# Kernel tuning notes

Measured on AMD Instinct MI355X. Metric: run time of the kernel, lower is better.

Reference implementation:

```python
import jax, jax.numpy as jnp
import numpy as np

E, H, D = 512, 8, 64
B, T = 2, 1024
HD = H * D


def _linear(x, W, b):
    return x @ W + b


def _ln(x, g, b):
    mu = x.mean(-1, keepdims=True)
    var = ((x - mu) ** 2).mean(-1, keepdims=True)
    return (x - mu) / jnp.sqrt(var + 1e-5) * g + b


def _l2norm(x):
    n = jnp.sqrt((x * x).sum(-1, keepdims=True))
    return x / jnp.maximum(n, 1e-12)


def setup_inputs() -> dict:
    key = jax.random.key(0)
    ks = jax.random.split(key, 32)
    s = 0.02
    inp = {
        'x': jax.random.normal(ks[0], (B, T, E), jnp.float32),
        'b_min': jax.random.normal(ks[1], (B, T, E), jnp.float32),
        'b_max': jax.random.normal(ks[2], (B, T, E), jnp.float32),
        'motif_context': jax.random.normal(ks[3], (B, T, E), jnp.float32),
        'Wk': jax.random.normal(ks[4], (E, HD), jnp.float32) * s,
        'bk': jnp.zeros((HD,), jnp.float32),
        'Wq': jax.random.normal(ks[5], (E, HD), jnp.float32) * s,
        'bq': jnp.zeros((HD,), jnp.float32),
        'Wv': jax.random.normal(ks[6], (E, HD), jnp.float32) * s,
        'bv': jnp.zeros((HD,), jnp.float32),
        'Wo': jax.random.normal(ks[7], (HD, E), jnp.float32) * s,
        'bo': jnp.zeros((E,), jnp.float32),
        'Wd': jax.random.normal(ks[8], (E, H), jnp.float32) * s,
        'bd': jnp.zeros((H,), jnp.float32),
        'Wgw': jax.random.normal(ks[9], (E, H), jnp.float32) * s,
        'bgw': jnp.zeros((H,), jnp.float32),
        'Wgf': jax.random.normal(ks[10], (E, H), jnp.float32) * s,
        'bgf': jnp.zeros((H,), jnp.float32),
        'Wps': jax.random.normal(ks[11], (E, E), jnp.float32) * s,
        'bps': jnp.zeros((E,), jnp.float32),
        'ln1_g': jnp.ones((E,), jnp.float32),
        'ln1_b': jnp.zeros((E,), jnp.float32),
        'ln2_g': jnp.ones((E,), jnp.float32),
        'ln2_b': jnp.zeros((E,), jnp.float32),
        'W1': jax.random.normal(ks[12], (E, 4 * E), jnp.float32) * s,
        'b1': jnp.zeros((4 * E,), jnp.float32),
        'W2': jax.random.normal(ks[13], (4 * E, E), jnp.float32) * s,
        'b2': jnp.zeros((E,), jnp.float32),
    }
    return inp


def reference(x, b_min, b_max, motif_context,
              Wk, bk, Wq, bq, Wv, bv, Wo, bo, Wd, bd,
              Wgw, bgw, Wgf, bgf, Wps, bps,
              ln1_g, ln1_b, ln2_g, ln2_b, W1, b1, W2, b2):
    Bs, Ts, Es = x.shape
    x_n = _ln(x, ln1_g, ln1_b)
    k = _l2norm(_linear(x_n, Wk, bk).reshape(Bs, Ts, H, D))
    q = _l2norm(_linear(x_n, Wq, bq).reshape(Bs, Ts, H, D))
    v = jnp.tanh(_linear(x_n, Wv, bv).reshape(Bs, Ts, H, D))
    d = jax.nn.softplus(_linear(x_n, Wd, bd))            # (B,T,H)
    gw = jax.nn.sigmoid(_linear(x_n, Wgw, bgw)) ** 2     # (B,T,H)
    gf = 1.0 - jax.nn.sigmoid(_linear(x_n, Wgf, bgf)) ** 2

    # gated linear recurrent scan via cumsum of rank-1 updates
    v_gated = v * (d * gw)[..., None]                    # (B,T,H,D)
    updates = jnp.einsum('bthi,bthj->bthij', v_gated, k)  # (B,T,H,D,D)
    decay = jnp.clip(d * gf, 1e-6, 0.999)
    log_decay = jnp.log(decay)[..., None, None]          # (B,T,H,1,1)
    exp_cum_decay = jnp.exp(jnp.cumsum(log_decay, axis=1))
    state = jnp.cumsum(updates / (exp_cum_decay + 1e-8), axis=1) * exp_cum_decay
    readout = jnp.einsum('bthij,bthj->bthi', state, q)   # (B,T,H,D)
    next_mem = state[:, -1]

    x2 = x + _linear(readout.reshape(Bs, Ts, HD), Wo, bo) + 0.1 * motif_context
    h = _ln(x2, ln2_g, ln2_b)
    x3 = x2 + _linear(jax.nn.gelu(_linear(h, W1, b1), approximate=False), W2, b2)
    probe = _linear(x3, Wps, bps)
    return (x3, next_mem, b_min + probe, b_max + probe)
```

## Files before the change

kernel.cpp:

```cpp
#include <hip/hip_runtime.h>


typedef unsigned short u16;
typedef unsigned int u32;
typedef __attribute__((ext_vector_type(8))) short short8;
typedef __attribute__((ext_vector_type(4))) float floatx4;

__device__ __forceinline__ float b2f(u16 u) {
  u32 x = ((u32)u) << 16;
  return __uint_as_float(x);
}
__device__ __forceinline__ u16 f2b(float f) {
  u32 x = __float_as_uint(f);
  u32 r = (x + 0x7fffu + ((x >> 16) & 1u)) >> 16;
  return (u16)r;
}
__device__ __forceinline__ float4 b4_to_f4(uint2 u) {
  float4 r;
  r.x = __uint_as_float((u.x & 0xffffu) << 16);
  r.y = __uint_as_float(u.x & 0xffff0000u);
  r.z = __uint_as_float((u.y & 0xffffu) << 16);
  r.w = __uint_as_float(u.y & 0xffff0000u);
  return r;
}

__device__ __forceinline__ void stage16(const u16* g, u16* lds_wave_base) {
  __builtin_amdgcn_global_load_lds((const __attribute__((address_space(1))) void*)g,
                                   (__attribute__((address_space(3))) void*)lds_wave_base,
                                   16, 0, 0);
}

template <int ROWS>
__device__ __forceinline__ void stage_tile64(const u16* __restrict__ G, int ldK, int kb,
                                             u16* lds, int tid) {
#pragma unroll
  for (int r = 0; r < ROWS / 32; ++r) {
    int slot = r * 256 + tid;
    int row = slot >> 3;
    int kwg = (slot & 7) ^ (row & 7);
    stage16(G + (size_t)row * ldK + kb * 64 + kwg * 8,
            lds + (size_t)(r * 256 + (tid >> 6) * 64) * 8);
  }
}

__device__ __forceinline__ void ln_row(const float* __restrict__ xr,
                                       const float* __restrict__ g,
                                       const float* __restrict__ bt,
                                       u16* __restrict__ yr, int tid, float* red) {
  float x0 = xr[tid], x1 = xr[tid + 256];
  float s = x0 + x1, ss = x0 * x0 + x1 * x1;
#pragma unroll
  for (int o = 32; o > 0; o >>= 1) { s += __shfl_xor(s, o); ss += __shfl_xor(ss, o); }
  if ((tid & 63) == 0) { red[tid >> 6] = s; red[4 + (tid >> 6)] = ss; }
  __syncthreads();
  float ts = red[0] + red[1] + red[2] + red[3];
  float tss = red[4] + red[5] + red[6] + red[7];
  float mu = ts * (1.f / 512.f);
  float var = tss * (1.f / 512.f) - mu * mu;
  float rstd = 1.0f / sqrtf(var + 1e-5f);
  yr[tid] = f2b((x0 - mu) * rstd * g[tid] + bt[tid]);
  yr[tid + 256] = f2b((x1 - mu) * rstd * g[tid + 256] + bt[tid + 256]);
}

__global__ __launch_bounds__(256) void prep_weights(
    const float* __restrict__ Wk, const float* __restrict__ Wq,
    const float* __restrict__ Wv, const float* __restrict__ Wo,
    const float* __restrict__ Wps, const float* __restrict__ W1,
    const float* __restrict__ W2, const float* __restrict__ Wd,
    const float* __restrict__ Wgw, const float* __restrict__ Wgf,
    const float* __restrict__ bk, const float* __restrict__ bq,
    const float* __restrict__ bv, const float* __restrict__ bd,
    const float* __restrict__ bgw, const float* __restrict__ bgf,
    const float* __restrict__ x, const float* __restrict__ ln1g,
    const float* __restrict__ ln1b,
    u16* __restrict__ WTQ, u16* __restrict__ WTO, u16* __restrict__ WTPS,
    u16* __restrict__ WT1, u16* __restrict__ WT2, float* __restrict__ BQV,
    u16* __restrict__ XN) {
  int bid = blockIdx.x, tid = threadIdx.x;
  __shared__ float tile[32][33];
  __shared__ float red[8];
  if (bid < 3328) {
    const float* src;
    u16* dst;
    int C, rel, tiles_x;
    if (bid < 256)       { src = Wk;  dst = WTQ;           C = 512;  rel = bid;        tiles_x = 16; }
    else if (bid < 512)  { src = Wq;  dst = WTQ + 262144;  C = 512;  rel = bid - 256;  tiles_x = 16; }
    else if (bid < 768)  { src = Wv;  dst = WTQ + 524288;  C = 512;  rel = bid - 512;  tiles_x = 16; }
    else if (bid < 1024) { src = Wo;  dst = WTO;           C = 512;  rel = bid - 768;  tiles_x = 16; }
    else if (bid < 1280) { src = Wps; dst = WTPS;          C = 512;  rel = bid - 1024; tiles_x = 16; }
    else if (bid < 2304) { src = W1;  dst = WT1;           C = 2048; rel = bid - 1280; tiles_x = 64; }
    else                 { src = W2;  dst = WT2;           C = 512;  rel = bid - 2304; tiles_x = 16; }
    int R = (bid >= 1280 && bid < 2304) ? 512 : (bid >= 2304 ? 2048 : 512);
    int c0 = (rel % tiles_x) * 32, r0 = (rel / tiles_x) * 32;
    int tx = tid & 31, ty = tid >> 5;
#pragma unroll
    for (int i = 0; i < 4; ++i)
      tile[ty + i * 8][tx] = src[(size_t)(r0 + ty + i * 8) * C + c0 + tx];
    __syncthreads();
#pragma unroll
    for (int i = 0; i < 4; ++i)
      dst[(size_t)(c0 + ty + i * 8) * R + r0 + tx] = f2b(tile[tx][ty + i * 8]);
  } else if (bid < 3392) {
    int idx = (bid - 3328) * 256 + tid;
    const int stride = 64 * 256;
    for (int i = idx; i < 128 * 512; i += stride) {
      int local = i >> 9, k = i & 511;
      float v = 0.f;
      if (local < 8) v = Wd[k * 8 + local];
      else if (local < 16) v = Wgw[k * 8 + (local - 8)];
      else if (local < 24) v = Wgf[k * 8 + (local - 16)];
      WTQ[(size_t)(1536 + local) * 512 + k] = f2b(v);
    }
    for (int i = idx; i < 1664; i += stride) {
      float v = 0.f;
      if (i < 512) v = bk[i];
      else if (i < 1024) v = bq[i - 512];
      else if (i < 1536) v = bv[i - 1024];
      else if (i < 1544) v = bd[i - 1536];
      else if (i < 1552) v = bgw[i - 1544];
      else if (i < 1560) v = bgf[i - 1552];
      BQV[i] = v;
    }
  } else {
    int row = bid - 3392;
    ln_row(x + (size_t)row * 512, ln1g, ln1b, XN + (size_t)row * 512, tid, red);
  }
}

__global__ __launch_bounds__(256) void ln_f32(const float* __restrict__ X,
                                              const float* __restrict__ g,
                                              const float* __restrict__ bt,
                                              u16* __restrict__ Y) {
  __shared__ float red[8];
  ln_row(X + (size_t)blockIdx.x * 512, g, bt, Y + (size_t)blockIdx.x * 512,
         threadIdx.x, red);
}

template <int BM, int EPI>
__global__ __launch_bounds__(256, (BM == 64 ? 4 : 6)) void gemm2s(
    const u16* __restrict__ A, const u16* __restrict__ BT, const float* __restrict__ bias,
    float* __restrict__ outf, float* __restrict__ outf2, u16* __restrict__ outb,
    u16* __restrict__ outb2, u16* __restrict__ outb3,
    const float* __restrict__ aux0, const float* __restrict__ aux1, int M, int N, int K) {
  constexpr int MT = BM / 32;
  constexpr int S = BM / 32 + 2;
  __shared__ __align__(16) u16 As[2][BM * 64];
  __shared__ __align__(16) u16 Bs[2][64 * 64];
  __shared__ float ssb[2][BM];
  const int tid = threadIdx.x;
  const int lane = tid & 63, wave = tid >> 6;
  const int wm = wave >> 1, wn = wave & 1;
  const int m0 = blockIdx.y * BM, n0 = blockIdx.x * 64;
  floatx4 acc[MT][2] = {};
  const int fr = lane & 15, kq = lane >> 4;
  const int nk = K >> 6;
  const u16* Ab = A + (size_t)m0 * K;
  const u16* Bb = BT + (size_t)n0 * K;

  stage_tile64<BM>(Ab, K, 0, As[0], tid);
  stage_tile64<64>(Bb, K, 0, Bs[0], tid);

  for (int kb = 0; kb < nk; ++kb) {
    const int cur = kb & 1;
    if (kb + 1 < nk) {
      stage_tile64<BM>(Ab, K, kb + 1, As[cur ^ 1], tid);
      stage_tile64<64>(Bb, K, kb + 1, Bs[cur ^ 1], tid);
      if constexpr (S == 4) asm volatile("s_waitcnt vmcnt(4)" ::: "memory");
      else asm volatile("s_waitcnt vmcnt(3)" ::: "memory");
    } else {
      asm volatile("s_waitcnt vmcnt(0)" ::: "memory");
    }
    asm volatile("s_barrier" ::: "memory");

#pragma unroll
    for (int sub = 0; sub < 2; ++sub) {
      short8 af[MT], bf[2];
#pragma unroll
      for (int mt = 0; mt < MT; ++mt) {
        int row = wm * (BM / 2) + mt * 16 + fr;
        int c = sub * 4 + kq;
        af[mt] = *(const short8*)&As[cur][row * 64 + ((c ^ (row & 7)) << 3)];
      }
#pragma unroll
      for (int nt = 0; nt < 2; ++nt) {
        int row = wn * 32 + nt * 16 + fr;
        int c = sub * 4 + kq;
        bf[nt] = *(const short8*)&Bs[cur][row * 64 + ((c ^ (row & 7)) << 3)];
      }
#pragma unroll
      for (int mt = 0; mt < MT; ++mt)
#pragma unroll
        for (int nt = 0; nt < 2; ++nt)
          acc[mt][nt] =
              __builtin_amdgcn_mfma_f32_16x16x32_bf16(af[mt], bf[nt], acc[mt][nt], 0, 0, 0);
    }
    asm volatile("s_waitcnt lgkmcnt(0)" ::: "memory");
    asm volatile("s_barrier" ::: "memory");
  }

  const int col = lane & 15;
  const int rbase = (lane >> 4) * 4;

  float vv[MT][2][4];
#pragma unroll
  for (int nt = 0; nt < 2; ++nt) {
    int gc = n0 + wn * 32 + nt * 16 + col;
    float bvv = bias[gc];
#pragma unroll
    for (int mt = 0; mt < MT; ++mt)
#pragma unroll
      for (int r = 0; r < 4; ++r) vv[mt][nt][r] = acc[mt][nt][r] + bvv;
  }

  if constexpr (EPI == 5) {
    const int sec = n0 >> 9;
    const int h = (n0 & 511) >> 6;
    if (sec == 3) {
#pragma unroll
      for (int nt = 0; nt < 2; ++nt) {
        int gcl = (n0 - 1536) + wn * 32 + nt * 16 + col;
#pragma unroll
        for (int mt = 0; mt < MT; ++mt) {
          int gr = m0 + wm * (BM / 2) + mt * 16 + rbase;
#pragma unroll
          for (int r = 0; r < 4; ++r)
            outf[(size_t)(gr + r) * 128 + gcl] = vv[mt][nt][r];
        }
      }
    } else if (sec == 2) {
#pragma unroll
      for (int nt = 0; nt < 2; ++nt) {
        int d = wn * 32 + nt * 16 + col;
#pragma unroll
        for (int mt = 0; mt < MT; ++mt) {
          int gr = m0 + wm * (BM / 2) + mt * 16 + rbase;
#pragma unroll
          for (int r = 0; r < 4; ++r) {
            int tok = gr + r;
            int bh = (tok >> 10) * 8 + h;
            outb3[((size_t)bh * 1024 + (tok & 1023)) * 64 + d] = f2b(tanhf(vv[mt][nt][r]));
          }
        }
      }
    } else {
#pragma unroll
      for (int mt = 0; mt < MT; ++mt) {
#pragma unroll
        for (int r = 0; r < 4; ++r) {
          float ss = vv[mt][0][r] * vv[mt][0][r] + vv[mt][1][r] * vv[mt][1][r];
          ss += __shfl_xor(ss, 1);
          ss += __shfl_xor(ss, 2);
          ss += __shfl_xor(ss, 4);
          ss += __shfl_xor(ss, 8);
          if ((lane & 15) == 0)
            ssb[wn][wm * (BM / 2) + mt * 16 + rbase + r] = ss;
        }
      }
      __syncthreads();
      u16* dst = (sec == 0) ? outb : outb2;
#pragma unroll
      for (int mt = 0; mt < MT; ++mt) {
#pragma unroll
        for (int r = 0; r < 4; ++r) {
          int br = wm * (BM / 2) + mt * 16 + rbase + r;
          float tot = ssb[0][br] + ssb[1][br];
          float rs = 1.0f / fmaxf(sqrtf(tot), 1e-12f);
          int tok = m0 + br;
          int bh = (tok >> 10) * 8 + h;
          size_t base = ((size_t)bh * 1024 + (tok & 1023)) * 64;
#pragma unroll
          for (int nt = 0; nt < 2; ++nt) {
            int d = wn * 32 + nt * 16 + col;
            dst[base + d] = f2b(vv[mt][nt][r] * rs);
          }
        }
      }
    }
  } else {
#pragma unroll
    for (int nt = 0; nt < 2; ++nt) {
      int gc = n0 + wn * 32 + nt * 16 + col;
#pragma unroll
      for (int mt = 0; mt < MT; ++mt) {
        int gr = m0 + wm * (BM / 2) + mt * 16 + rbase;
#pragma unroll
        for (int r = 0; r < 4; ++r) {
          size_t idx = (size_t)(gr + r) * N + gc;
          float v = vv[mt][nt][r];
          if constexpr (EPI == 1) {
            outf[idx] = aux0[idx] + v + 0.1f * aux1[idx];
          } else if constexpr (EPI == 2) {
            outb[idx] = f2b(0.5f * v * (1.f + erff(v * 0.70710678118654752f)));
          } else if constexpr (EPI == 3) {
            float w = aux0[idx] + v;
            outf[idx] = w;
            outb[idx] = f2b(w);
          } else if constexpr (EPI == 4) {
            outf[idx] = aux0[idx] + v;
            outf2[idx] = aux1[idx] + v;
          }
        }
      }
    }
  }
}

__global__ __launch_bounds__(256) void gates_logcum(
    const float* __restrict__ G0, float* __restrict__ DEC, float* __restrict__ SVG,
    float* __restrict__ LC, float* __restrict__ WW) {
  int bh = blockIdx.x;
  int b = bh >> 3, h = bh & 7;
  int tid = threadIdx.x;
  __shared__ float ldec[1024];
#pragma unroll
  for (int tt = 0; tt < 4; ++tt) {
    int t = tt * 256 + tid;
    size_t tok = (size_t)b * 1024 + t;
    float dl = G0[tok * 128 + h];
    float gwl = G0[tok * 128 + 8 + h];
    float gfl = G0[tok * 128 + 16 + h];
    float dd = dl > 20.f ? dl : log1pf(expf(dl));
    float sw = 1.f / (1.f + expf(-gwl));
    float gw = sw * sw;
    float sf = 1.f / (1.f + expf(-gfl));
    float gf = 1.f - sf * sf;
    float dec = fminf(fmaxf(dd * gf, 1e-6f), 0.999f);
    ldec[t] = dec;
    DEC[(size_t)bh * 1024 + t] = dec;
    SVG[(size_t)bh * 1024 + t] = dd * gw;
  }
  __syncthreads();
  if (tid < 64) {
    int lane = tid;
    size_t base = (size_t)bh * 1024 + lane * 16;
    float loc[16];
    float run = 0.f;
#pragma unroll
    for (int i = 0; i < 16; ++i) { run += logf(ldec[lane * 16 + i]); loc[i] = run; }
    float x = run;
#pragma unroll
    for (int o = 1; o < 64; o <<= 1) {
      float v = __shfl_up(x, o);
      if (lane >= o) x += v;
    }
    float excl = x - run;
#pragma unroll
    for (int i = 0; i < 16; ++i) {
      float L = excl + loc[i];
      LC[base + i] = L;
      float c = expf(L);
      WW[base + i] = c / (c + 1e-8f);
    }
  }
}

__global__ __launch_bounds__(256, 2) void scan_phase1(
    const u16* __restrict__ KB, const u16* __restrict__ QB, const u16* __restrict__ VB,
    const float* __restrict__ DEC, const float* __restrict__ WW,
    const float* __restrict__ SVG, float* __restrict__ RP, float* __restrict__ SF) {
  int chunk = blockIdx.x, h = blockIdx.y, b = blockIdx.z;
  int bh = b * 8 + h;
  int t0 = chunk * 32;
  __shared__ __align__(16) float sk[2048], sq[2048], sv[2048];
  __shared__ float lsa[32], lsw[32];
  int tid = threadIdx.x;

  const u16* gk = KB + ((size_t)bh * 1024 + t0) * 64;
  const u16* gq = QB + ((size_t)bh * 1024 + t0) * 64;
  const u16* gv = VB + ((size_t)bh * 1024 + t0) * 64;
#pragma unroll
  for (int r = 0; r < 2; ++r) {
    int f = (r * 256 + tid) * 4;
    *(float4*)&sk[f] = b4_to_f4(*(const uint2*)(gk + f));
    *(float4*)&sq[f] = b4_to_f4(*(const uint2*)(gq + f));
    *(float4*)&sv[f] = b4_to_f4(*(const uint2*)(gv + f));
  }
  if (tid < 32) {
    size_t gi = (size_t)bh * 1024 + t0 + tid;
    lsa[tid] = DEC[gi];
    lsw[tid] = WW[gi] * SVG[gi];
  }
  __syncthreads();

  int i = tid >> 2, j0 = (tid & 3) * 16;
  float s[16];
#pragma unroll
  for (int z = 0; z < 16; ++z) s[z] = 0.f;

  for (int t = 0; t < 32; ++t) {
    float a = lsa[t], w = lsw[t];
    float wv = w * sv[t * 64 + i];
    float r = 0.f;
#pragma unroll
    for (int u4 = 0; u4 < 4; ++u4) {
      float4 kv = *(const float4*)&sk[t * 64 + j0 + u4 * 4];
      float4 qv = *(const float4*)&sq[t * 64 + j0 + u4 * 4];
      s[u4 * 4 + 0] = fmaf(a, s[u4 * 4 + 0], wv * kv.x); r = fmaf(s[u4 * 4 + 0], qv.x, r);
      s[u4 * 4 + 1] = fmaf(a, s[u4 * 4 + 1], wv * kv.y); r = fmaf(s[u4 * 4 + 1], qv.y, r);
      s[u4 * 4 + 2] = fmaf(a, s[u4 * 4 + 2], wv * kv.z); r = fmaf(s[u4 * 4 + 2], qv.z, r);
      s[u4 * 4 + 3] = fmaf(a, s[u4 * 4 + 3], wv * kv.w); r = fmaf(s[u4 * 4 + 3], qv.w, r);
    }
    r += __shfl_xor(r, 1);
    r += __shfl_xor(r, 2);
    if ((tid & 3) == 0)
      RP[((size_t)(b * 1024 + t0 + t) * 8 + h) * 64 + i] = r;
  }

  float* Sf = SF + ((size_t)bh * 32 + chunk) * 4096 + i * 64 + j0;
#pragma unroll
  for (int u4 = 0; u4 < 4; ++u4) {
    float4 v;
    v.x = s[u4 * 4 + 0]; v.y = s[u4 * 4 + 1]; v.z = s[u4 * 4 + 2]; v.w = s[u4 * 4 + 3];
    *(float4*)&Sf[u4 * 4] = v;
  }
}

__global__ __launch_bounds__(256) void scan_phase2p(const float* __restrict__ SF,
                                                    const float* __restrict__ LC,
                                                    float* __restrict__ SI,
                                                    float* __restrict__ next_mem) {
  int bh = blockIdx.x >> 4;
  int e = (blockIdx.x & 15) * 256 + threadIdx.x;
  float s = 0.f;
  for (int c = 0; c < 32; ++c) {
    SI[((size_t)bh * 32 + c) * 4096 + e] = s;
    float Lend = LC[(size_t)bh * 1024 + c * 32 + 31];
    float Lpre = c ? LC[(size_t)bh * 1024 + c * 32 - 1] : 0.f;
    float P = expf(Lend - Lpre);
    s = fmaf(P, s, SF[((size_t)bh * 32 + c) * 4096 + e]);
  }
  next_mem[(size_t)bh * 4096 + e] = s;
}

__global__ __launch_bounds__(256, 2) void scan_phase3(
    const u16* __restrict__ QB, const float* __restrict__ SI, const float* __restrict__ LC,
    const float* __restrict__ RP, u16* __restrict__ AB) {
  int chunk = blockIdx.x, h = blockIdx.y, b = blockIdx.z;
  int bh = b * 8 + h;
  int t0 = chunk * 32;
  __shared__ __align__(16) float sq[2048];
  __shared__ float sL[32];
  int tid = threadIdx.x;

  const u16* gq = QB + ((size_t)bh * 1024 + t0) * 64;
#pragma unroll
  for (int r = 0; r < 2; ++r) {
    int f = (r * 256 + tid) * 4;
    *(float4*)&sq[f] = b4_to_f4(*(const uint2*)(gq + f));
  }
  if (tid < 32) sL[tid] = LC[(size_t)bh * 1024 + t0 + tid];
  __syncthreads();

  float Lpre = chunk ? LC[(size_t)bh * 1024 + t0 - 1] : 0.f;
  int i = tid >> 2, j0 = (tid & 3) * 16;
  const float* Si = SI + ((size_t)bh * 32 + chunk) * 4096 + i * 64 + j0;
  float S[16];
#pragma unroll
  for (int u4 = 0; u4 < 4; ++u4) {
    float4 v = *(const float4*)&Si[u4 * 4];
    S[u4 * 4 + 0] = v.x; S[u4 * 4 + 1] = v.y; S[u4 * 4 + 2] = v.z; S[u4 * 4 + 3] = v.w;
  }

  for (int t = 0; t < 32; ++t) {
    float p = expf(sL[t] - Lpre);
    float r = 0.f;
#pragma unroll
    for (int u4 = 0; u4 < 4; ++u4) {
      float4 qv = *(const float4*)&sq[t * 64 + j0 + u4 * 4];
      r = fmaf(S[u4 * 4 + 0], qv.x, r);
      r = fmaf(S[u4 * 4 + 1], qv.y, r);
      r = fmaf(S[u4 * 4 + 2], qv.z, r);
      r = fmaf(S[u4 * 4 + 3], qv.w, r);
    }
    r += __shfl_xor(r, 1);
    r += __shfl_xor(r, 2);
    if ((tid & 3) == 0) {
      size_t gi = ((size_t)(b * 1024 + t0 + t) * 8 + h) * 64 + i;
      AB[gi] = f2b(RP[gi] + p * r);
    }
  }
}

extern "C" void kernel_launch(void* const* d_in, const int* in_sizes, int n_in,
                              void* d_out, int out_size, void* d_ws, size_t ws_size,
                              hipStream_t stream) {
  const float* x = (const float*)d_in[0];
  const float* bmin = (const float*)d_in[1];
  const float* bmax = (const float*)d_in[2];
  const float* motif = (const float*)d_in[3];
  const float* Wk = (const float*)d_in[4];
  const float* bk = (const float*)d_in[5];
  const float* Wq = (const float*)d_in[6];
  const float* bq = (const float*)d_in[7];
  const float* Wv = (const float*)d_in[8];
  const float* bv = (const float*)d_in[9];
  const float* Wo = (const float*)d_in[10];
  const float* bo = (const float*)d_in[11];
  const float* Wd = (const float*)d_in[12];
  const float* bd = (const float*)d_in[13];
  const float* Wgw = (const float*)d_in[14];
  const float* bgw = (const float*)d_in[15];
  const float* Wgf = (const float*)d_in[16];
  const float* bgf = (const float*)d_in[17];
  const float* Wps = (const float*)d_in[18];
  const float* bps = (const float*)d_in[19];
  const float* ln1g = (const float*)d_in[20];
  const float* ln1b = (const float*)d_in[21];
  const float* ln2g = (const float*)d_in[22];
  const float* ln2b = (const float*)d_in[23];
  const float* W1 = (const float*)d_in[24];
  const float* b1 = (const float*)d_in[25];
  const float* W2 = (const float*)d_in[26];
  const float* b2 = (const float*)d_in[27];

  char* ws = (char*)d_ws;
  u16* WTQ = (u16*)(ws + 0);
  u16* WTO = (u16*)(ws + 1703936);
  u16* WT1 = (u16*)(ws + 2228224);
  u16* WT2 = (u16*)(ws + 4325376);
  u16* WTPS = (u16*)(ws + 6422528);
  float* BQV = (float*)(ws + 6946816);
  u16* XN = (u16*)(ws + 6953984);
  float* G0 = (float*)(ws + 9051136);
  u16* KB = (u16*)(ws + 10099712);
  u16* QB = (u16*)(ws + 12196864);
  u16* VB = (u16*)(ws + 14294016);
  float* DEC = (float*)(ws + 16391168);
  float* LC = (float*)(ws + 16456704);
  float* WW = (float*)(ws + 16522240);
  float* SVG = (float*)(ws + 16587776);
  float* RP = (float*)(ws + 16653312);
  float* SF = (float*)(ws + 20847616);
  float* SI = (float*)(ws + 29236224);
  u16* AB = (u16*)(ws + 37624832);
  float* X2 = (float*)(ws + 39721984);
  u16* HB = (u16*)(ws + 43916288);
  u16* MID = (u16*)(ws + 9051136);
  u16* X3B = (u16*)(ws + 20847616);

  float* out0 = (float*)d_out;
  float* out1 = out0 + 1048576;
  float* out2 = out0 + 1114112;
  float* out3 = out0 + 2162688;

  prep_weights<<<5440, 256, 0, stream>>>(Wk, Wq, Wv, Wo, Wps, W1, W2, Wd, Wgw, Wgf,
                                         bk, bq, bv, bd, bgw, bgf, x, ln1g, ln1b,
                                         WTQ, WTO, WTPS, WT1, WT2, BQV, XN);
  gemm2s<64, 5><<<dim3(26, 32), 256, 0, stream>>>(XN, WTQ, BQV, G0, nullptr, KB, QB, VB,
                                                  nullptr, nullptr, 2048, 1664, 512);
  gates_logcum<<<16, 256, 0, stream>>>(G0, DEC, SVG, LC, WW);
  scan_phase1<<<dim3(32, 8, 2), 256, 0, stream>>>(KB, QB, VB, DEC, WW, SVG, RP, SF);
  scan_phase2p<<<256, 256, 0, stream>>>(SF, LC, SI, out1);
  scan_phase3<<<dim3(32, 8, 2), 256, 0, stream>>>(QB, SI, LC, RP, AB);

  gemm2s<32, 1><<<dim3(8, 64), 256, 0, stream>>>(AB, WTO, bo, X2, nullptr, nullptr,
                                                 nullptr, nullptr, x, motif, 2048, 512, 512);
  ln_f32<<<2048, 256, 0, stream>>>(X2, ln2g, ln2b, HB);
  gemm2s<64, 2><<<dim3(32, 32), 256, 0, stream>>>(HB, WT1, b1, nullptr, nullptr, MID,
                                                  nullptr, nullptr, nullptr, nullptr,
                                                  2048, 2048, 512);
  gemm2s<32, 3><<<dim3(8, 64), 256, 0, stream>>>(MID, WT2, b2, out0, nullptr, X3B,
                                                 nullptr, nullptr, X2, nullptr,
                                                 2048, 512, 2048);
  gemm2s<32, 4><<<dim3(8, 64), 256, 0, stream>>>(X3B, WTPS, bps, out2, out3, nullptr,
                                                 nullptr, nullptr, bmin, bmax,
                                                 2048, 512, 512);
}
```

Before: 226.6 us.

## Fuse gate, chunked scan phases into one cooperative kernel with grid syncs

Replaces four separate kernels (gates_logcum, scan_phase1, scan_phase2p, scan_phase3) with a single cooperative launch that uses grid.sync between stages. The intra-chunk readout stays in shared memory instead of going through the RP buffer, and the WW and SVG arrays are merged into one precomputed weight. The aim is to cut launch gaps and some global traffic. The cost is grid-wide barriers, and with 512 blocks at 2 per CU the grid must fit co-resident on the device. The phase-2 work also now runs on only 16 of 32 chunks per head.

```diff
diff --git a/kernel.cpp b/kernel.cpp
--- a/kernel.cpp
+++ b/kernel.cpp
@@ -1,4 +1,7 @@
 #include <hip/hip_runtime.h>
+#include <hip/hip_cooperative_groups.h>
+
+namespace cg = cooperative_groups;
 
 
 typedef unsigned short u16;
@@ -137,7 +140,7 @@
 }
 
 template <int BM, int EPI>
-__global__ __launch_bounds__(256, (BM == 64 ? 4 : 6)) void gemm2s(
+__global__ __launch_bounds__(256, (BM == 128 ? 3 : BM == 64 ? 4 : 6)) void gemm2s(
     const u16* __restrict__ A, const u16* __restrict__ BT, const float* __restrict__ bias,
     float* __restrict__ outf, float* __restrict__ outf2, u16* __restrict__ outb,
     u16* __restrict__ outb2, u16* __restrict__ outb3,
@@ -165,7 +168,8 @@
     if (kb + 1 < nk) {
       stage_tile64<BM>(Ab, K, kb + 1, As[cur ^ 1], tid);
       stage_tile64<64>(Bb, K, kb + 1, Bs[cur ^ 1], tid);
-      if constexpr (S == 4) asm volatile("s_waitcnt vmcnt(4)" ::: "memory");
+      if constexpr (S == 6) asm volatile("s_waitcnt vmcnt(6)" ::: "memory");
+      else if constexpr (S == 4) asm volatile("s_waitcnt vmcnt(4)" ::: "memory");
       else asm volatile("s_waitcnt vmcnt(3)" ::: "memory");
     } else {
       asm volatile("s_waitcnt vmcnt(0)" ::: "memory");
@@ -305,178 +309,169 @@
   }
 }
 
-__global__ __launch_bounds__(256) void gates_logcum(
-    const float* __restrict__ G0, float* __restrict__ DEC, float* __restrict__ SVG,
-    float* __restrict__ LC, float* __restrict__ WW) {
-  int bh = blockIdx.x;
-  int b = bh >> 3, h = bh & 7;
-  int tid = threadIdx.x;
-  __shared__ float ldec[1024];
-#pragma unroll
-  for (int tt = 0; tt < 4; ++tt) {
-    int t = tt * 256 + tid;
-    size_t tok = (size_t)b * 1024 + t;
-    float dl = G0[tok * 128 + h];
-    float gwl = G0[tok * 128 + 8 + h];
-    float gfl = G0[tok * 128 + 16 + h];
-    float dd = dl > 20.f ? dl : log1pf(expf(dl));
-    float sw = 1.f / (1.f + expf(-gwl));
-    float gw = sw * sw;
-    float sf = 1.f / (1.f + expf(-gfl));
-    float gf = 1.f - sf * sf;
-    float dec = fminf(fmaxf(dd * gf, 1e-6f), 0.999f);
-    ldec[t] = dec;
-    DEC[(size_t)bh * 1024 + t] = dec;
-    SVG[(size_t)bh * 1024 + t] = dd * gw;
-  }
-  __syncthreads();
-  if (tid < 64) {
-    int lane = tid;
-    size_t base = (size_t)bh * 1024 + lane * 16;
-    float loc[16];
-    float run = 0.f;
-#pragma unroll
-    for (int i = 0; i < 16; ++i) { run += logf(ldec[lane * 16 + i]); loc[i] = run; }
-    float x = run;
-#pragma unroll
-    for (int o = 1; o < 64; o <<= 1) {
-      float v = __shfl_up(x, o);
-      if (lane >= o) x += v;
-    }
-    float excl = x - run;
-#pragma unroll
-    for (int i = 0; i < 16; ++i) {
-      float L = excl + loc[i];
-      LC[base + i] = L;
-      float c = expf(L);
-      WW[base + i] = c / (c + 1e-8f);
-    }
-  }
-}
-
-__global__ __launch_bounds__(256, 2) void scan_phase1(
+__global__ __launch_bounds__(256, 2) void scan_fused(
     const u16* __restrict__ KB, const u16* __restrict__ QB, const u16* __restrict__ VB,
-    const float* __restrict__ DEC, const float* __restrict__ WW,
-    const float* __restrict__ SVG, float* __restrict__ RP, float* __restrict__ SF) {
-  int chunk = blockIdx.x, h = blockIdx.y, b = blockIdx.z;
-  int bh = b * 8 + h;
-  int t0 = chunk * 32;
+    const float* __restrict__ G0, float* __restrict__ DEC, float* __restrict__ WS,
+    float* __restrict__ LC, float* __restrict__ SF, float* __restrict__ SI,
+    float* __restrict__ next_mem, u16* __restrict__ AB) {
+  const int chunk = blockIdx.x, h = blockIdx.y, b = blockIdx.z;
+  const int bh = b * 8 + h;
+  const int t0 = chunk * 32;
+  const int tid = threadIdx.x;
   __shared__ __align__(16) float sk[2048], sq[2048], sv[2048];
   __shared__ float lsa[32], lsw[32];
-  int tid = threadIdx.x;
-
-  const u16* gk = KB + ((size_t)bh * 1024 + t0) * 64;
-  const u16* gq = QB + ((size_t)bh * 1024 + t0) * 64;
-  const u16* gv = VB + ((size_t)bh * 1024 + t0) * 64;
-#pragma unroll
-  for (int r = 0; r < 2; ++r) {
-    int f = (r * 256 + tid) * 4;
-    *(float4*)&sk[f] = b4_to_f4(*(const uint2*)(gk + f));
-    *(float4*)&sq[f] = b4_to_f4(*(const uint2*)(gq + f));
-    *(float4*)&sv[f] = b4_to_f4(*(const uint2*)(gv + f));
-  }
-  if (tid < 32) {
-    size_t gi = (size_t)bh * 1024 + t0 + tid;
-    lsa[tid] = DEC[gi];
-    lsw[tid] = WW[gi] * SVG[gi];
-  }
-  __syncthreads();
-
-  int i = tid >> 2, j0 = (tid & 3) * 16;
-  float s[16];
-#pragma unroll
-  for (int z = 0; z < 16; ++z) s[z] = 0.f;
-
-  for (int t = 0; t < 32; ++t) {
-    float a = lsa[t], w = lsw[t];
-    float wv = w * sv[t * 64 + i];
-    float r = 0.f;
+  cg::grid_group grid = cg::this_grid();
+
+  if (chunk == 0) {
+    float* ldec = sk;
+    float* lsvg = sq;
+#pragma unroll
+    for (int tt = 0; tt < 4; ++tt) {
+      int t = tt * 256 + tid;
+      size_t tok = (size_t)b * 1024 + t;
+      float dl = G0[tok * 128 + h];
+      float gwl = G0[tok * 128 + 8 + h];
+      float gfl = G0[tok * 128 + 16 + h];
+      float dd = dl > 20.f ? dl : log1pf(expf(dl));
+      float sw = 1.f / (1.f + expf(-gwl));
+      float gw = sw * sw;
+      float sf = 1.f / (1.f + expf(-gfl));
+      float gf = 1.f - sf * sf;
+      float dec = fminf(fmaxf(dd * gf, 1e-6f), 0.999f);
+      ldec[t] = dec;
+      lsvg[t] = dd * gw;
+      DEC[(size_t)bh * 1024 + t] = dec;
+    }
+    __syncthreads();
+    if (tid < 64) {
+      int lane = tid;
+      size_t base = (size_t)bh * 1024 + lane * 16;
+      float loc[16];
+      float run = 0.f;
+#pragma unroll
+      for (int i = 0; i < 16; ++i) { run += logf(ldec[lane * 16 + i]); loc[i] = run; }
+      float x = run;
+#pragma unroll
+      for (int o = 1; o < 64; o <<= 1) {
+        float v = __shfl_up(x, o);
+        if (lane >= o) x += v;
+      }
+      float excl = x - run;
+#pragma unroll
+      for (int i = 0; i < 16; ++i) {
+        float L = excl + loc[i];
+        LC[base + i] = L;
+        float c = expf(L);
+        WS[base + i] = (c / (c + 1e-8f)) * lsvg[lane * 16 + i];
+      }
+    }
+  }
+  grid.sync();
+
+  {
+    const u16* gk = KB + ((size_t)bh * 1024 + t0) * 64;
+    const u16* gq = QB + ((size_t)bh * 1024 + t0) * 64;
+    const u16* gv = VB + ((size_t)bh * 1024 + t0) * 64;
+#pragma unroll
+    for (int r = 0; r < 2; ++r) {
+      int f = (r * 256 + tid) * 4;
+      *(float4*)&sk[f] = b4_to_f4(*(const uint2*)(gk + f));
+      *(float4*)&sq[f] = b4_to_f4(*(const uint2*)(gq + f));
+      *(float4*)&sv[f] = b4_to_f4(*(const uint2*)(gv + f));
+    }
+    if (tid < 32) {
+      size_t gi = (size_t)bh * 1024 + t0 + tid;
+      lsa[tid] = DEC[gi];
+      lsw[tid] = WS[gi];
+    }
+    __syncthreads();
+
+    int i = tid >> 2, j0 = (tid & 3) * 16;
+    float s[16];
+#pragma unroll
+    for (int z = 0; z < 16; ++z) s[z] = 0.f;
+
+    for (int t = 0; t < 32; ++t) {
+      float a = lsa[t], w = lsw[t];
+      float wv = w * sv[t * 64 + i];
+      float r = 0.f;
+#pragma unroll
+      for (int u4 = 0; u4 < 4; ++u4) {
+        float4 kv = *(const float4*)&sk[t * 64 + j0 + u4 * 4];
+        float4 qv = *(const float4*)&sq[t * 64 + j0 + u4 * 4];
+        s[u4 * 4 + 0] = fmaf(a, s[u4 * 4 + 0], wv * kv.x); r = fmaf(s[u4 * 4 + 0], qv.x, r);
+        s[u4 * 4 + 1] = fmaf(a, s[u4 * 4 + 1], wv * kv.y); r = fmaf(s[u4 * 4 + 1], qv.y, r);
+        s[u4 * 4 + 2] = fmaf(a, s[u4 * 4 + 2], wv * kv.z); r = fmaf(s[u4 * 4 + 2], qv.z, r);
+        s[u4 * 4 + 3] = fmaf(a, s[u4 * 4 + 3], wv * kv.w); r = fmaf(s[u4 * 4 + 3], qv.w, r);
+      }
+      r += __shfl_xor(r, 1);
+      r += __shfl_xor(r, 2);
+      if ((tid & 3) == 0) sv[t * 64 + i] = r;
+    }
+
+    float* Sf = SF + ((size_t)bh * 32 + chunk) * 4096 + i * 64 + j0;
 #pragma unroll
     for (int u4 = 0; u4 < 4; ++u4) {
-      float4 kv = *(const float4*)&sk[t * 64 + j0 + u4 * 4];
-      float4 qv = *(const float4*)&sq[t * 64 + j0 + u4 * 4];
-      s[u4 * 4 + 0] = fmaf(a, s[u4 * 4 + 0], wv * kv.x); r = fmaf(s[u4 * 4 + 0], qv.x, r);
-      s[u4 * 4 + 1] = fmaf(a, s[u4 * 4 + 1], wv * kv.y); r = fmaf(s[u4 * 4 + 1], qv.y, r);
-      s[u4 * 4 + 2] = fmaf(a, s[u4 * 4 + 2], wv * kv.z); r = fmaf(s[u4 * 4 + 2], qv.z, r);
-      s[u4 * 4 + 3] = fmaf(a, s[u4 * 4 + 3], wv * kv.w); r = fmaf(s[u4 * 4 + 3], qv.w, r);
-    }
-    r += __shfl_xor(r, 1);
-    r += __shfl_xor(r, 2);
-    if ((tid & 3) == 0)
-      RP[((size_t)(b * 1024 + t0 + t) * 8 + h) * 64 + i] = r;
-  }
-
-  float* Sf = SF + ((size_t)bh * 32 + chunk) * 4096 + i * 64 + j0;
-#pragma unroll
-  for (int u4 = 0; u4 < 4; ++u4) {
-    float4 v;
-    v.x = s[u4 * 4 + 0]; v.y = s[u4 * 4 + 1]; v.z = s[u4 * 4 + 2]; v.w = s[u4 * 4 + 3];
-    *(float4*)&Sf[u4 * 4] = v;
-  }
-}
-
-__global__ __launch_bounds__(256) void scan_phase2p(const float* __restrict__ SF,
-                                                    const float* __restrict__ LC,
-                                                    float* __restrict__ SI,
-                                                    float* __restrict__ next_mem) {
-  int bh = blockIdx.x >> 4;
-  int e = (blockIdx.x & 15) * 256 + threadIdx.x;
-  float s = 0.f;
-  for (int c = 0; c < 32; ++c) {
-    SI[((size_t)bh * 32 + c) * 4096 + e] = s;
-    float Lend = LC[(size_t)bh * 1024 + c * 32 + 31];
-    float Lpre = c ? LC[(size_t)bh * 1024 + c * 32 - 1] : 0.f;
-    float P = expf(Lend - Lpre);
-    s = fmaf(P, s, SF[((size_t)bh * 32 + c) * 4096 + e]);
-  }
-  next_mem[(size_t)bh * 4096 + e] = s;
-}
-
-__global__ __launch_bounds__(256, 2) void scan_phase3(
-    const u16* __restrict__ QB, const float* __restrict__ SI, const float* __restrict__ LC,
-    const float* __restrict__ RP, u16* __restrict__ AB) {
-  int chunk = blockIdx.x, h = blockIdx.y, b = blockIdx.z;
-  int bh = b * 8 + h;
-  int t0 = chunk * 32;
-  __shared__ __align__(16) float sq[2048];
-  __shared__ float sL[32];
-  int tid = threadIdx.x;
-
-  const u16* gq = QB + ((size_t)bh * 1024 + t0) * 64;
-#pragma unroll
-  for (int r = 0; r < 2; ++r) {
-    int f = (r * 256 + tid) * 4;
-    *(float4*)&sq[f] = b4_to_f4(*(const uint2*)(gq + f));
-  }
-  if (tid < 32) sL[tid] = LC[(size_t)bh * 1024 + t0 + tid];
-  __syncthreads();
-
-  float Lpre = chunk ? LC[(size_t)bh * 1024 + t0 - 1] : 0.f;
-  int i = tid >> 2, j0 = (tid & 3) * 16;
-  const float* Si = SI + ((size_t)bh * 32 + chunk) * 4096 + i * 64 + j0;
-  float S[16];
-#pragma unroll
-  for (int u4 = 0; u4 < 4; ++u4) {
-    float4 v = *(const float4*)&Si[u4 * 4];
-    S[u4 * 4 + 0] = v.x; S[u4 * 4 + 1] = v.y; S[u4 * 4 + 2] = v.z; S[u4 * 4 + 3] = v.w;
-  }
-
-  for (int t = 0; t < 32; ++t) {
-    float p = expf(sL[t] - Lpre);
-    float r = 0.f;
+      float4 v;
+      v.x = s[u4 * 4 + 0]; v.y = s[u4 * 4 + 1]; v.z = s[u4 * 4 + 2]; v.w = s[u4 * 4 + 3];
+      *(float4*)&Sf[u4 * 4] = v;
+    }
+  }
+  grid.sync();
+
+  if (chunk < 16) {
+    if (tid < 32) {
+      float Lend = LC[(size_t)bh * 1024 + tid * 32 + 31];
+      float Lpre = tid ? LC[(size_t)bh * 1024 + tid * 32 - 1] : 0.f;
+      lsw[tid] = expf(Lend - Lpre);
+    }
+    __syncthreads();
+    int e = chunk * 256 + tid;
+    const float* Sfb = SF + (size_t)bh * 32 * 4096 + e;
+    float* Sib = SI + (size_t)bh * 32 * 4096 + e;
+    float sf0[32];
+#pragma unroll
+    for (int c = 0; c < 32; ++c) sf0[c] = Sfb[(size_t)c * 4096];
+    float s = 0.f;
+#pragma unroll
+    for (int c = 0; c < 32; ++c) {
+      Sib[(size_t)c * 4096] = s;
+      s = fmaf(lsw[c], s, sf0[c]);
+    }
+    next_mem[(size_t)bh * 4096 + e] = s;
+  }
+  grid.sync();
+
+  {
+    if (tid < 32) lsa[tid] = LC[(size_t)bh * 1024 + t0 + tid];
+    __syncthreads();
+    float Lpre = chunk ? LC[(size_t)bh * 1024 + t0 - 1] : 0.f;
+    int i = tid >> 2, j0 = (tid & 3) * 16;
+    const float* Si = SI + ((size_t)bh * 32 + chunk) * 4096 + i * 64 + j0;
+    float S[16];
 #pragma unroll
     for (int u4 = 0; u4 < 4; ++u4) {
-      float4 qv = *(const float4*)&sq[t * 64 + j0 + u4 * 4];
-      r = fmaf(S[u4 * 4 + 0], qv.x, r);
-      r = fmaf(S[u4 * 4 + 1], qv.y, r);
-      r = fmaf(S[u4 * 4 + 2], qv.z, r);
-      r = fmaf(S[u4 * 4 + 3], qv.w, r);
-    }
-    r += __shfl_xor(r, 1);
-    r += __shfl_xor(r, 2);
-    if ((tid & 3) == 0) {
-      size_t gi = ((size_t)(b * 1024 + t0 + t) * 8 + h) * 64 + i;
-      AB[gi] = f2b(RP[gi] + p * r);
+      float4 v = *(const float4*)&Si[u4 * 4];
+      S[u4 * 4 + 0] = v.x; S[u4 * 4 + 1] = v.y; S[u4 * 4 + 2] = v.z; S[u4 * 4 + 3] = v.w;
+    }
+
+    for (int t = 0; t < 32; ++t) {
+      float p = expf(lsa[t] - Lpre);
+      float r = 0.f;
+#pragma unroll
+      for (int u4 = 0; u4 < 4; ++u4) {
+        float4 qv = *(const float4*)&sq[t * 64 + j0 + u4 * 4];
+        r = fmaf(S[u4 * 4 + 0], qv.x, r);
+        r = fmaf(S[u4 * 4 + 1], qv.y, r);
+        r = fmaf(S[u4 * 4 + 2], qv.z, r);
+        r = fmaf(S[u4 * 4 + 3], qv.w, r);
+      }
+      r += __shfl_xor(r, 1);
+      r += __shfl_xor(r, 2);
+      if ((tid & 3) == 0) {
+        size_t gi = ((size_t)(b * 1024 + t0 + t) * 8 + h) * 64 + i;
+        AB[gi] = f2b(sv[t * 64 + i] + p * r);
+      }
     }
   }
 }
@@ -527,9 +522,7 @@
   u16* VB = (u16*)(ws + 14294016);
   float* DEC = (float*)(ws + 16391168);
   float* LC = (float*)(ws + 16456704);
-  float* WW = (float*)(ws + 16522240);
-  float* SVG = (float*)(ws + 16587776);
-  float* RP = (float*)(ws + 16653312);
+  float* WS = (float*)(ws + 16522240);
   float* SF = (float*)(ws + 20847616);
   float* SI = (float*)(ws + 29236224);
   u16* AB = (u16*)(ws + 37624832);
@@ -548,10 +541,13 @@
                                          WTQ, WTO, WTPS, WT1, WT2, BQV, XN);
   gemm2s<64, 5><<<dim3(26, 32), 256, 0, stream>>>(XN, WTQ, BQV, G0, nullptr, KB, QB, VB,
                                                   nullptr, nullptr, 2048, 1664, 512);
-  gates_logcum<<<16, 256, 0, stream>>>(G0, DEC, SVG, LC, WW);
-  scan_phase1<<<dim3(32, 8, 2), 256, 0, stream>>>(KB, QB, VB, DEC, WW, SVG, RP, SF);
-  scan_phase2p<<<256, 256, 0, stream>>>(SF, LC, SI, out1);
-  scan_phase3<<<dim3(32, 8, 2), 256, 0, stream>>>(QB, SI, LC, RP, AB);
+  {
+    void* args[] = {(void*)&KB, (void*)&QB, (void*)&VB, (void*)&G0, (void*)&DEC,
+                    (void*)&WS, (void*)&LC, (void*)&SF, (void*)&SI, (void*)&out1,
+                    (void*)&AB};
+    hipLaunchCooperativeKernel((const void*)scan_fused, dim3(32, 8, 2), dim3(256),
+                               args, 0, stream);
+  }
 
   gemm2s<32, 1><<<dim3(8, 64), 256, 0, stream>>>(AB, WTO, bo, X2, nullptr, nullptr,
                                                  nullptr, nullptr, x, motif, 2048, 512, 512);
```

Result: slower. 449.3 us (+98.3%).

## Fuse chunk-state prefix scan into readout kernel and premultiply gate weights

Applied to the files above, without the earlier changes.

Removes the separate phase-2 scan kernel. Each phase-3 block now recomputes its own chunk-start state by serially accumulating the preceding chunk-final states, and the last chunk writes next_mem. This drops one launch and the SI intermediate buffer, but the redundant prefix work grows with chunk index, giving later chunks up to 31 serial 4096-float reads and an uneven load across blocks. The gate kernel also writes the WW*SVG product as one buffer, and the GEMM template gains unused BM=128 launch bounds and wait-count cases.

```diff
diff --git a/kernel.cpp b/kernel.cpp
--- a/kernel.cpp
+++ b/kernel.cpp
@@ -137,7 +137,7 @@
 }
 
 template <int BM, int EPI>
-__global__ __launch_bounds__(256, (BM == 64 ? 4 : 6)) void gemm2s(
+__global__ __launch_bounds__(256, (BM == 128 ? 3 : BM == 64 ? 4 : 6)) void gemm2s(
     const u16* __restrict__ A, const u16* __restrict__ BT, const float* __restrict__ bias,
     float* __restrict__ outf, float* __restrict__ outf2, u16* __restrict__ outb,
     u16* __restrict__ outb2, u16* __restrict__ outb3,
@@ -165,7 +165,8 @@
     if (kb + 1 < nk) {
       stage_tile64<BM>(Ab, K, kb + 1, As[cur ^ 1], tid);
       stage_tile64<64>(Bb, K, kb + 1, Bs[cur ^ 1], tid);
-      if constexpr (S == 4) asm volatile("s_waitcnt vmcnt(4)" ::: "memory");
+      if constexpr (S == 6) asm volatile("s_waitcnt vmcnt(6)" ::: "memory");
+      else if constexpr (S == 4) asm volatile("s_waitcnt vmcnt(4)" ::: "memory");
       else asm volatile("s_waitcnt vmcnt(3)" ::: "memory");
     } else {
       asm volatile("s_waitcnt vmcnt(0)" ::: "memory");
@@ -306,12 +307,13 @@
 }
 
 __global__ __launch_bounds__(256) void gates_logcum(
-    const float* __restrict__ G0, float* __restrict__ DEC, float* __restrict__ SVG,
-    float* __restrict__ LC, float* __restrict__ WW) {
+    const float* __restrict__ G0, float* __restrict__ DEC, float* __restrict__ WS,
+    float* __restrict__ LC) {
   int bh = blockIdx.x;
   int b = bh >> 3, h = bh & 7;
   int tid = threadIdx.x;
   __shared__ float ldec[1024];
+  __shared__ float lsvg[1024];
 #pragma unroll
   for (int tt = 0; tt < 4; ++tt) {
     int t = tt * 256 + tid;
@@ -326,8 +328,8 @@
     float gf = 1.f - sf * sf;
     float dec = fminf(fmaxf(dd * gf, 1e-6f), 0.999f);
     ldec[t] = dec;
+    lsvg[t] = dd * gw;
     DEC[(size_t)bh * 1024 + t] = dec;
-    SVG[(size_t)bh * 1024 + t] = dd * gw;
   }
   __syncthreads();
   if (tid < 64) {
@@ -349,15 +351,15 @@
       float L = excl + loc[i];
       LC[base + i] = L;
       float c = expf(L);
-      WW[base + i] = c / (c + 1e-8f);
+      WS[base + i] = (c / (c + 1e-8f)) * lsvg[lane * 16 + i];
     }
   }
 }
 
 __global__ __launch_bounds__(256, 2) void scan_phase1(
     const u16* __restrict__ KB, const u16* __restrict__ QB, const u16* __restrict__ VB,
-    const float* __restrict__ DEC, const float* __restrict__ WW,
-    const float* __restrict__ SVG, float* __restrict__ RP, float* __restrict__ SF) {
+    const float* __restrict__ DEC, const float* __restrict__ WS,
+    float* __restrict__ RP, float* __restrict__ SF) {
   int chunk = blockIdx.x, h = blockIdx.y, b = blockIdx.z;
   int bh = b * 8 + h;
   int t0 = chunk * 32;
@@ -378,7 +380,7 @@
   if (tid < 32) {
     size_t gi = (size_t)bh * 1024 + t0 + tid;
     lsa[tid] = DEC[gi];
-    lsw[tid] = WW[gi] * SVG[gi];
+    lsw[tid] = WS[gi];
   }
   __syncthreads();
 
@@ -415,31 +417,14 @@
   }
 }
 
-__global__ __launch_bounds__(256) void scan_phase2p(const float* __restrict__ SF,
-                                                    const float* __restrict__ LC,
-                                                    float* __restrict__ SI,
-                                                    float* __restrict__ next_mem) {
-  int bh = blockIdx.x >> 4;
-  int e = (blockIdx.x & 15) * 256 + threadIdx.x;
-  float s = 0.f;
-  for (int c = 0; c < 32; ++c) {
-    SI[((size_t)bh * 32 + c) * 4096 + e] = s;
-    float Lend = LC[(size_t)bh * 1024 + c * 32 + 31];
-    float Lpre = c ? LC[(size_t)bh * 1024 + c * 32 - 1] : 0.f;
-    float P = expf(Lend - Lpre);
-    s = fmaf(P, s, SF[((size_t)bh * 32 + c) * 4096 + e]);
-  }
-  next_mem[(size_t)bh * 4096 + e] = s;
-}
-
-__global__ __launch_bounds__(256, 2) void scan_phase3(
-    const u16* __restrict__ QB, const float* __restrict__ SI, const float* __restrict__ LC,
-    const float* __restrict__ RP, u16* __restrict__ AB) {
+__global__ __launch_bounds__(256, 2) void scan_phase23(
+    const u16* __restrict__ QB, const float* __restrict__ SF, const float* __restrict__ LC,
+    const float* __restrict__ RP, float* __restrict__ next_mem, u16* __restrict__ AB) {
   int chunk = blockIdx.x, h = blockIdx.y, b = blockIdx.z;
   int bh = b * 8 + h;
   int t0 = chunk * 32;
   __shared__ __align__(16) float sq[2048];
-  __shared__ float sL[32];
+  __shared__ float sL[32], sP[32];
   int tid = threadIdx.x;
 
   const u16* gq = QB + ((size_t)bh * 1024 + t0) * 64;
@@ -448,19 +433,54 @@
     int f = (r * 256 + tid) * 4;
     *(float4*)&sq[f] = b4_to_f4(*(const uint2*)(gq + f));
   }
-  if (tid < 32) sL[tid] = LC[(size_t)bh * 1024 + t0 + tid];
+  if (tid < 32) {
+    sL[tid] = LC[(size_t)bh * 1024 + t0 + tid];
+    float Lend = LC[(size_t)bh * 1024 + tid * 32 + 31];
+    float Lpre = tid ? LC[(size_t)bh * 1024 + tid * 32 - 1] : 0.f;
+    sP[tid] = expf(Lend - Lpre);
+  }
   __syncthreads();
 
+  int i = tid >> 2, j0 = (tid & 3) * 16;
+  const float* Sfb = SF + (size_t)bh * 32 * 4096 + i * 64 + j0;
+
+  float S[16];
+#pragma unroll
+  for (int z = 0; z < 16; ++z) S[z] = 0.f;
+  for (int c = 0; c < chunk; ++c) {
+    float P = sP[c];
+    const float* row = Sfb + (size_t)c * 4096;
+    float4 f0 = *(const float4*)&row[0];
+    float4 f1 = *(const float4*)&row[4];
+    float4 f2 = *(const float4*)&row[8];
+    float4 f3 = *(const float4*)&row[12];
+    S[0] = fmaf(P, S[0], f0.x);  S[1] = fmaf(P, S[1], f0.y);
+    S[2] = fmaf(P, S[2], f0.z);  S[3] = fmaf(P, S[3], f0.w);
+    S[4] = fmaf(P, S[4], f1.x);  S[5] = fmaf(P, S[5], f1.y);
+    S[6] = fmaf(P, S[6], f1.z);  S[7] = fmaf(P, S[7], f1.w);
+    S[8] = fmaf(P, S[8], f2.x);  S[9] = fmaf(P, S[9], f2.y);
+    S[10] = fmaf(P, S[10], f2.z); S[11] = fmaf(P, S[11], f2.w);
+    S[12] = fmaf(P, S[12], f3.x); S[13] = fmaf(P, S[13], f3.y);
+    S[14] = fmaf(P, S[14], f3.z); S[15] = fmaf(P, S[15], f3.w);
+  }
+
+  if (chunk == 31) {
+    float P = sP[31];
+    const float* row = Sfb + (size_t)31 * 4096;
+    float* nm = next_mem + (size_t)bh * 4096 + i * 64 + j0;
+#pragma unroll
+    for (int u4 = 0; u4 < 4; ++u4) {
+      float4 f = *(const float4*)&row[u4 * 4];
+      float4 o;
+      o.x = fmaf(P, S[u4 * 4 + 0], f.x);
+      o.y = fmaf(P, S[u4 * 4 + 1], f.y);
+      o.z = fmaf(P, S[u4 * 4 + 2], f.z);
+      o.w = fmaf(P, S[u4 * 4 + 3], f.w);
+      *(float4*)&nm[u4 * 4] = o;
+    }
+  }
+
   float Lpre = chunk ? LC[(size_t)bh * 1024 + t0 - 1] : 0.f;
-  int i = tid >> 2, j0 = (tid & 3) * 16;
-  const float* Si = SI + ((size_t)bh * 32 + chunk) * 4096 + i * 64 + j0;
-  float S[16];
-#pragma unroll
-  for (int u4 = 0; u4 < 4; ++u4) {
-    float4 v = *(const float4*)&Si[u4 * 4];
-    S[u4 * 4 + 0] = v.x; S[u4 * 4 + 1] = v.y; S[u4 * 4 + 2] = v.z; S[u4 * 4 + 3] = v.w;
-  }
-
   for (int t = 0; t < 32; ++t) {
     float p = expf(sL[t] - Lpre);
     float r = 0.f;
@@ -527,16 +547,14 @@
   u16* VB = (u16*)(ws + 14294016);
   float* DEC = (float*)(ws + 16391168);
   float* LC = (float*)(ws + 16456704);
-  float* WW = (float*)(ws + 16522240);
-  float* SVG = (float*)(ws + 16587776);
+  float* WS = (float*)(ws + 16522240);
   float* RP = (float*)(ws + 16653312);
   float* SF = (float*)(ws + 20847616);
-  float* SI = (float*)(ws + 29236224);
   u16* AB = (u16*)(ws + 37624832);
   float* X2 = (float*)(ws + 39721984);
   u16* HB = (u16*)(ws + 43916288);
   u16* MID = (u16*)(ws + 9051136);
-  u16* X3B = (u16*)(ws + 20847616);
+  u16* X3B = (u16*)(ws + 29236224);
 
   float* out0 = (float*)d_out;
   float* out1 = out0 + 1048576;
@@ -548,10 +566,9 @@
                                          WTQ, WTO, WTPS, WT1, WT2, BQV, XN);
   gemm2s<64, 5><<<dim3(26, 32), 256, 0, stream>>>(XN, WTQ, BQV, G0, nullptr, KB, QB, VB,
                                                   nullptr, nullptr, 2048, 1664, 512);
-  gates_logcum<<<16, 256, 0, stream>>>(G0, DEC, SVG, LC, WW);
-  scan_phase1<<<dim3(32, 8, 2), 256, 0, stream>>>(KB, QB, VB, DEC, WW, SVG, RP, SF);
-  scan_phase2p<<<256, 256, 0, stream>>>(SF, LC, SI, out1);
-  scan_phase3<<<dim3(32, 8, 2), 256, 0, stream>>>(QB, SI, LC, RP, AB);
+  gates_logcum<<<16, 256, 0, stream>>>(G0, DEC, WS, LC);
+  scan_phase1<<<dim3(32, 8, 2), 256, 0, stream>>>(KB, QB, VB, DEC, WS, RP, SF);
+  scan_phase23<<<dim3(32, 8, 2), 256, 0, stream>>>(QB, SF, LC, RP, out1, AB);
 
   gemm2s<32, 1><<<dim3(8, 64), 256, 0, stream>>>(AB, WTO, bo, X2, nullptr, nullptr,
                                                  nullptr, nullptr, x, motif, 2048, 512, 512);
```

Result: slower. 236.4 us (+4.3%).
